# Performance work log

Measured on AMD Instinct MI355X. Metric: run time of the kernel, lower is better.

## Reference

```python
import jax, jax.numpy as jnp
import numpy as np

PATCH_LEN = 16
PATCH_STRIDE = 8
DIM = 512
NUM_HEADS = 8
HEAD_DIM = DIM // NUM_HEADS
NUM_LAYERS = 4
MLP_HIDDEN = 4 * DIM
ROPE_BASE = 10000.0
LN_EPS = 1e-5


def setup_inputs() -> dict:
    key = jax.random.key(0)
    ks = jax.random.split(key, 20)
    B, T, C = 4, 8192, 7
    s = 0.02
    inp = {
        "x": jax.random.normal(ks[0], (B, T, C), dtype=jnp.float32),
        "W_emb": jax.random.normal(ks[1], (PATCH_LEN * C, DIM), dtype=jnp.float32) * s,
        "b_emb": jnp.zeros((DIM,), jnp.float32),
        "ln1_g": jnp.ones((NUM_LAYERS, DIM), jnp.float32),
        "ln1_b": jnp.zeros((NUM_LAYERS, DIM), jnp.float32),
        "W_qkv": jax.random.normal(ks[2], (NUM_LAYERS, DIM, 3 * DIM), dtype=jnp.float32) * s,
        "b_qkv": jnp.zeros((NUM_LAYERS, 3 * DIM), jnp.float32),
        "W_proj": jax.random.normal(ks[3], (NUM_LAYERS, DIM, DIM), dtype=jnp.float32) * s,
        "b_proj": jnp.zeros((NUM_LAYERS, DIM), jnp.float32),
        "ln2_g": jnp.ones((NUM_LAYERS, DIM), jnp.float32),
        "ln2_b": jnp.zeros((NUM_LAYERS, DIM), jnp.float32),
        "W_mlp1": jax.random.normal(ks[4], (NUM_LAYERS, DIM, MLP_HIDDEN), dtype=jnp.float32) * s,
        "b_mlp1": jnp.zeros((NUM_LAYERS, MLP_HIDDEN), jnp.float32),
        "W_mlp2": jax.random.normal(ks[5], (NUM_LAYERS, MLP_HIDDEN, DIM), dtype=jnp.float32) * s,
        "b_mlp2": jnp.zeros((NUM_LAYERS, DIM), jnp.float32),
        "lnf_g": jnp.ones((DIM,), jnp.float32),
        "lnf_b": jnp.zeros((DIM,), jnp.float32),
    }
    return inp


def _layer_norm(x, g, b):
    mu = jnp.mean(x, axis=-1, keepdims=True)
    var = jnp.mean(jnp.square(x - mu), axis=-1, keepdims=True)
    return (x - mu) * jax.lax.rsqrt(var + LN_EPS) * g + b


def _rotate_half(x):
    x1, x2 = jnp.split(x, 2, axis=-1)
    return jnp.concatenate((-x2, x1), axis=-1)


def _rope_cos_sin(seq_len):
    t = jnp.arange(seq_len, dtype=jnp.float32)
    inv_freq = 1.0 / (ROPE_BASE ** (jnp.arange(0, HEAD_DIM, 2, dtype=jnp.float32) / HEAD_DIM))
    freqs = jnp.outer(t, inv_freq)                      # [L, hd/2]
    emb = jnp.concatenate((freqs, freqs), axis=-1)      # [L, hd]
    return jnp.cos(emb), jnp.sin(emb)


def _forward(x, W_emb, b_emb, ln1_g, ln1_b, W_qkv, b_qkv, W_proj, b_proj,
             ln2_g, ln2_b, W_mlp1, b_mlp1, W_mlp2, b_mlp2, lnf_g, lnf_b):
    B, T, C = x.shape
    n = (T - PATCH_LEN) // PATCH_STRIDE + 1
    # torch unfold: [B, n, C, patch_len], then flattened as (C, patch_len)
    idx = jnp.arange(n)[:, None] * PATCH_STRIDE + jnp.arange(PATCH_LEN)[None, :]  # [n, P]
    patches = x[:, idx, :]                              # [B, n, P, C]
    patches = patches.transpose(0, 1, 3, 2).reshape(B, n, C * PATCH_LEN)
    emb = patches @ W_emb + b_emb                       # [B, n, D]

    cos, sin = _rope_cos_sin(n)                         # [n, hd]
    cos = cos[None, None, :, :]
    sin = sin[None, None, :, :]
    scale = HEAD_DIM ** -0.5

    h = emb
    for i in range(NUM_LAYERS):
        # --- attention ---
        y = _layer_norm(h, ln1_g[i], ln1_b[i])
        qkv = (y @ W_qkv[i] + b_qkv[i]).reshape(B, n, 3, NUM_HEADS, HEAD_DIM)
        qkv = qkv.transpose(2, 0, 3, 1, 4)              # [3, B, H, n, hd]
        q, k, v = qkv[0], qkv[1], qkv[2]
        q = q * cos + _rotate_half(q) * sin
        k = k * cos + _rotate_half(k) * sin
        attn = jax.nn.softmax(jnp.einsum('bhqd,bhkd->bhqk', q, k) * scale, axis=-1)
        o = jnp.einsum('bhqk,bhkd->bhqd', attn, v)      # [B, H, n, hd]
        o = o.transpose(0, 2, 1, 3).reshape(B, n, DIM)
        h = h + (o @ W_proj[i] + b_proj[i])
        # --- mlp ---
        y = _layer_norm(h, ln2_g[i], ln2_b[i])
        y = jax.nn.gelu(y @ W_mlp1[i] + b_mlp1[i], approximate=False)
        h = h + (y @ W_mlp2[i] + b_mlp2[i])

    x_out = _layer_norm(h, lnf_g, lnf_b)
    return emb, x_out


def reference(x, W_emb, b_emb, ln1_g, ln1_b, W_qkv, b_qkv, W_proj, b_proj,
              ln2_g, ln2_b, W_mlp1, b_mlp1, W_mlp2, b_mlp2, lnf_g, lnf_b):
    return _forward(x, W_emb, b_emb, ln1_g, ln1_b, W_qkv, b_qkv, W_proj, b_proj,
                    ln2_g, ln2_b, W_mlp1, b_mlp1, W_mlp2, b_mlp2, lnf_g, lnf_b)
```

## Files before the change

### kernel.cpp

```cpp
#include <hip/hip_runtime.h>
#include <hip/hip_bf16.h>
#include <math.h>

#define B_SZ 4
#define T_LEN 8192
#define C_IN 7
#define NPATCH 1023
#define DIM 512
#define NH 8
#define HD 64
#define NLAYERS 4
#define MLP_HID 2048
#define M_ROWS (B_SZ * NPATCH)
#define KEMB 128
#define LN_EPS 1e-5f

typedef __attribute__((ext_vector_type(8))) short short8;
typedef __attribute__((ext_vector_type(4))) float float4v;

static __device__ __forceinline__ unsigned short f2bf(float f) {
  __hip_bfloat16 h = __float2bfloat16(f);
  return *reinterpret_cast<unsigned short*>(&h);
}
static __device__ __forceinline__ float bf2f(unsigned short u) {
  return __uint_as_float(((unsigned)u) << 16);
}

__global__ __launch_bounds__(256) void patch_kernel(
    const float* __restrict__ x, unsigned short* __restrict__ Pm) {
  int idx = blockIdx.x * 256 + threadIdx.x;
  if (idx >= M_ROWS * KEMB) return;
  int row = idx >> 7, c = idx & 127;
  float v = 0.f;
  if (c < 112) {
    int b = row / NPATCH, i = row - b * NPATCH;
    int ci = c >> 4, p = c & 15;
    v = x[((size_t)b * T_LEN + (size_t)i * 8 + p) * C_IN + ci];
  }
  Pm[idx] = f2bf(v);
}

__global__ __launch_bounds__(256) void wemb_cvt_kernel(
    const float* __restrict__ W, unsigned short* __restrict__ Wt) {
  int idx = blockIdx.x * 256 + threadIdx.x;
  if (idx >= DIM * KEMB) return;
  int n = idx >> 7, k = idx & 127;
  float v = (k < 112) ? W[(size_t)k * DIM + n] : 0.f;
  Wt[idx] = f2bf(v);
}

template <bool BF>
__global__ __launch_bounds__(256) void ln_kernel(
    const float* __restrict__ in, const float* __restrict__ g,
    const float* __restrict__ bb, void* __restrict__ outv, int M) {
  int row = blockIdx.x * 4 + (threadIdx.x >> 6);
  if (row >= M) return;
  int lane = threadIdx.x & 63;
  const float* xr = in + (size_t)row * DIM;
  float v[8];
  float s = 0.f;
  #pragma unroll
  for (int k = 0; k < 8; ++k) { v[k] = xr[lane + 64 * k]; s += v[k]; }
  #pragma unroll
  for (int off = 32; off; off >>= 1) s += __shfl_down(s, off);
  s = __shfl(s, 0);
  float mu = s * (1.f / DIM);
  float q = 0.f;
  #pragma unroll
  for (int k = 0; k < 8; ++k) { float d = v[k] - mu; q = fmaf(d, d, q); }
  #pragma unroll
  for (int off = 32; off; off >>= 1) q += __shfl_down(q, off);
  q = __shfl(q, 0);
  float rstd = rsqrtf(q * (1.f / DIM) + LN_EPS);
  #pragma unroll
  for (int k = 0; k < 8; ++k) {
    int d = lane + 64 * k;
    float r = (v[k] - mu) * rstd * g[d] + bb[d];
    if (BF)
      ((unsigned short*)outv)[(size_t)row * DIM + d] = f2bf(r);
    else
      ((float*)outv)[(size_t)row * DIM + d] = r;
  }
}

__global__ __launch_bounds__(256) void wcvt_kernel(
    const float* __restrict__ W, unsigned short* __restrict__ Wt, int K, int N) {
  __shared__ float tile[32][33];
  int n0 = blockIdx.x * 32, k0 = blockIdx.y * 32, L = blockIdx.z;
  const float* Ws = W + (size_t)L * K * N;
  unsigned short* Wd = Wt + (size_t)L * K * N;
  int tx = threadIdx.x & 31, ty = threadIdx.x >> 5;
  #pragma unroll
  for (int i = 0; i < 4; ++i)
    tile[ty + i * 8][tx] = Ws[(size_t)(k0 + ty + i * 8) * N + n0 + tx];
  __syncthreads();
  #pragma unroll
  for (int i = 0; i < 4; ++i)
    Wd[(size_t)(n0 + ty + i * 8) * K + k0 + tx] = f2bf(tile[tx][ty + i * 8]);
}

__global__ __launch_bounds__(256) void rope_tab_kernel(float2* __restrict__ tab) {
  int idx = blockIdx.x * 256 + threadIdx.x;
  if (idx >= NPATCH * 32) return;
  int i = idx >> 5, j = idx & 31;
  float inv = powf(10000.0f, -(float)j * (1.0f / 32.0f));
  float sn, cs;
  sincosf((float)i * inv, &sn, &cs);
  tab[idx] = make_float2(cs, sn);
}

template <int TM, int TN, int EPI>
__global__ __launch_bounds__(256) void mfma_gemm(
    const unsigned short* __restrict__ A, const unsigned short* __restrict__ Bt,
    const float* __restrict__ bias, const float* __restrict__ res,
    float* __restrict__ Cf, float* __restrict__ Cf2,
    unsigned short* __restrict__ Cb, const float2* __restrict__ rtab,
    int M, int N, int K) {
  constexpr int WM = TM / 2, WN = TN / 2;
  constexpr int NI = WM / 16, NJ = WN / 16;
  constexpr int ACH = TM * 4;
  constexpr int TCH = (TM + TN) * 4;
  constexpr int CH = TCH / 256;
  __shared__ __align__(16) unsigned short As[2][TM][40];
  __shared__ __align__(16) unsigned short Bs[2][TN][40];
  const int bm = blockIdx.y * TM;
  const int bn = blockIdx.x * TN;
  const int tid = threadIdx.x;
  const int lane = tid & 63, wave = tid >> 6;
  const int quad = lane >> 4, l16 = lane & 15;
  const int wm = (wave & 1) * WM;
  const int wn = (wave >> 1) * WN;

  float4v acc[NI][NJ];
  #pragma unroll
  for (int i = 0; i < NI; ++i)
    #pragma unroll
    for (int j = 0; j < NJ; ++j)
      acc[i][j] = (float4v){0.f, 0.f, 0.f, 0.f};

  uint4 pr[CH];
  auto load_regs = [&](int kk) {
    #pragma unroll
    for (int it = 0; it < CH; ++it) {
      int c = tid + it * 256;
      if (c < ACH) {
        int row = c >> 2, ch = (c & 3) * 8;
        int gm = bm + row;
        pr[it] = make_uint4(0u, 0u, 0u, 0u);
        if (gm < M) pr[it] = *(const uint4*)(A + (size_t)gm * K + kk + ch);
      } else {
        int c2 = c - ACH;
        int row = c2 >> 2, ch = (c2 & 3) * 8;
        pr[it] = *(const uint4*)(Bt + (size_t)(bn + row) * K + kk + ch);
      }
    }
  };

  load_regs(0);
  int buf = 0;
  for (int k0 = 0; k0 < K; k0 += 32, buf ^= 1) {
    #pragma unroll
    for (int it = 0; it < CH; ++it) {
      int c = tid + it * 256;
      if (c < ACH)
        *(uint4*)&As[buf][c >> 2][(c & 3) * 8] = pr[it];
      else {
        int c2 = c - ACH;
        *(uint4*)&Bs[buf][c2 >> 2][(c2 & 3) * 8] = pr[it];
      }
    }
    if (k0 + 32 < K) load_regs(k0 + 32);
    __syncthreads();
    short8 af[NI], bfr[NJ];
    #pragma unroll
    for (int i = 0; i < NI; ++i)
      af[i] = *(const short8*)&As[buf][wm + i * 16 + l16][quad * 8];
    #pragma unroll
    for (int j = 0; j < NJ; ++j)
      bfr[j] = *(const short8*)&Bs[buf][wn + j * 16 + l16][quad * 8];
    __builtin_amdgcn_s_setprio(1);
    #pragma unroll
    for (int i = 0; i < NI; ++i)
      #pragma unroll
      for (int j = 0; j < NJ; ++j)
        acc[i][j] = __builtin_amdgcn_mfma_f32_16x16x32_bf16(
            af[i], bfr[j], acc[i][j], 0, 0, 0);
    __builtin_amdgcn_s_setprio(0);
  }

  if (EPI == 6) {
    const int sec = (bn + wn) >> 9;
    #pragma unroll
    for (int i = 0; i < NI; ++i) {
      int gm0 = bm + wm + i * 16 + quad * 4;
      #pragma unroll
      for (int r = 0; r < 4; ++r) {
        int gm = gm0 + r;
        if (gm >= M) continue;
        size_t rowoff = (size_t)gm * N;
        if (sec < 2) {
          int ip = gm; if (ip >= 2046) ip -= 2046; if (ip >= 1023) ip -= 1023;
          float sc = (sec == 0) ? 0.125f : 1.f;
          #pragma unroll
          for (int j = 0; j < NJ / 2; ++j) {
            int gn = bn + wn + j * 16 + l16;
            float v0 = acc[i][j][r] + bias[gn];
            float v1 = acc[i][j + NJ / 2][r] + bias[gn + 32];
            float2 t = rtab[ip * 32 + j * 16 + l16];
            Cb[rowoff + gn]      = f2bf((v0 * t.x - v1 * t.y) * sc);
            Cb[rowoff + gn + 32] = f2bf((v1 * t.x + v0 * t.y) * sc);
          }
        } else {
          #pragma unroll
          for (int j = 0; j < NJ; ++j) {
            int gn = bn + wn + j * 16 + l16;
            Cb[rowoff + gn] = f2bf(acc[i][j][r] + bias[gn]);
          }
        }
      }
    }
    return;
  }

  #pragma unroll
  for (int j = 0; j < NJ; ++j) {
    int gn = bn + wn + j * 16 + l16;
    float bv = bias[gn];
    #pragma unroll
    for (int i = 0; i < NI; ++i) {
      int gm0 = bm + wm + i * 16 + quad * 4;
      #pragma unroll
      for (int r = 0; r < 4; ++r) {
        int gm = gm0 + r;
        if (gm < M) {
          float v = acc[i][j][r] + bv;
          size_t off = (size_t)gm * N + gn;
          if (EPI == 1) {
            Cf[off] = v + res[off];
          } else if (EPI == 2) {
            Cb[off] = f2bf(0.5f * v * (1.f + erff(v * 0.70710678118f)));
          } else if (EPI == 3) {
            Cb[off] = f2bf(v);
          } else {
            Cf[off] = v;
            Cf2[off] = v;
          }
        }
      }
    }
  }
}

#define APITCH 72

__global__ __launch_bounds__(256) void attn_kernel(
    const unsigned short* __restrict__ qkvb, unsigned short* __restrict__ o) {
  const int bid = blockIdx.x;
  const int xcd = bid & 7, slot = bid >> 3;
  const int qt0 = (slot & 15) * 64;
  const int gh = xcd + 8 * (slot >> 4);
  const int h = gh & 7, b = gh >> 3;

  const int tid = threadIdx.x;
  const int lane = tid & 63, wave = tid >> 6;
  const int quad = lane >> 4, l16 = lane & 15;

  __shared__ __align__(16) unsigned short Qs[64][APITCH];
  __shared__ __align__(16) unsigned short Ks[2][64][APITCH];
  __shared__ __align__(16) unsigned short Vt[2][HD][APITCH];
  __shared__ __align__(16) unsigned short Ps[4][16][APITCH];

  const int sr = tid >> 2;
  const int sc0 = (tid & 3) * 16;

  {
    int qi = qt0 + sr;
    uint4 a = make_uint4(0u, 0u, 0u, 0u), b2 = a;
    if (qi < NPATCH) {
      const uint4* src = (const uint4*)(qkvb + (size_t)(b * NPATCH + qi) * (3 * DIM) + h * HD + sc0);
      a = src[0]; b2 = src[1];
    }
    *(uint4*)&Qs[sr][sc0] = a;
    *(uint4*)&Qs[sr][sc0 + 8] = b2;
  }

  uint4 pk0, pk1;
  auto load_k = [&](int j0) {
    pk0 = pk1 = make_uint4(0u, 0u, 0u, 0u);
    int j = j0 + sr;
    if (j < NPATCH) {
      const unsigned short* kb = qkvb + (size_t)(b * NPATCH + j) * (3 * DIM) + DIM + h * HD;
      pk0 = *(const uint4*)(kb + sc0);
      pk1 = *(const uint4*)(kb + sc0 + 8);
    }
  };

  const int kp = tid & 31, dg = tid >> 5;
  uint4 pv0, pv1;
  auto load_v = [&](int j0) {
    pv0 = pv1 = make_uint4(0u, 0u, 0u, 0u);
    int j = j0 + 2 * kp;
    const unsigned short* vb = qkvb + (size_t)(b * NPATCH + j) * (3 * DIM) + 2 * DIM + h * HD + dg * 8;
    if (j < NPATCH)     pv0 = *(const uint4*)vb;
    if (j + 1 < NPATCH) pv1 = *(const uint4*)(vb + 3 * DIM);
  };

  load_k(0);
  load_v(0);
  __syncthreads();

  short8 aq0 = *(const short8*)&Qs[wave * 16 + l16][quad * 8];
  short8 aq1 = *(const short8*)&Qs[wave * 16 + l16][32 + quad * 8];

  float4v accO[4];
  #pragma unroll
  for (int j2 = 0; j2 < 4; ++j2) accO[j2] = (float4v){0.f, 0.f, 0.f, 0.f};
  float m_run[4] = {-1e30f, -1e30f, -1e30f, -1e30f};
  float lp[4] = {0.f, 0.f, 0.f, 0.f};

  int buf = 0;
  for (int j0 = 0; j0 < NPATCH; j0 += 64, buf ^= 1) {
    {
      *(uint4*)&Ks[buf][sr][sc0] = pk0;
      *(uint4*)&Ks[buf][sr][sc0 + 8] = pk1;
      unsigned short va[8], vb8[8];
      *(uint4*)&va[0] = pv0;
      *(uint4*)&vb8[0] = pv1;
      #pragma unroll
      for (int u = 0; u < 8; ++u) {
        unsigned pk = (unsigned)va[u] | ((unsigned)vb8[u] << 16);
        *(unsigned*)&Vt[buf][dg * 8 + u][2 * kp] = pk;
      }
    }
    __syncthreads();

    if (j0 + 64 < NPATCH) { load_k(j0 + 64); load_v(j0 + 64); }

    float4v s[4];
    __builtin_amdgcn_s_setprio(1);
    #pragma unroll
    for (int j = 0; j < 4; ++j) {
      s[j] = (float4v){0.f, 0.f, 0.f, 0.f};
      short8 bk0 = *(const short8*)&Ks[buf][j * 16 + l16][quad * 8];
      short8 bk1 = *(const short8*)&Ks[buf][j * 16 + l16][32 + quad * 8];
      s[j] = __builtin_amdgcn_mfma_f32_16x16x32_bf16(aq0, bk0, s[j], 0, 0, 0);
      s[j] = __builtin_amdgcn_mfma_f32_16x16x32_bf16(aq1, bk1, s[j], 0, 0, 0);
    }
    __builtin_amdgcn_s_setprio(0);

    float mx[4];
    #pragma unroll
    for (int r = 0; r < 4; ++r)
      mx[r] = fmaxf(fmaxf(s[0][r], s[1][r]), fmaxf(s[2][r], s[3][r]));
    #pragma unroll
    for (int mask = 1; mask < 16; mask <<= 1)
      #pragma unroll
      for (int r = 0; r < 4; ++r)
        mx[r] = fmaxf(mx[r], __shfl_xor(mx[r], mask));
    float gmax = fmaxf(fmaxf(mx[0] - m_run[0], mx[1] - m_run[1]),
                       fmaxf(mx[2] - m_run[2], mx[3] - m_run[3]));
    if (!__all(gmax <= 8.f)) {
      #pragma unroll
      for (int r = 0; r < 4; ++r) {
        float mnew = fmaxf(m_run[r], mx[r]);
        float al = __expf(m_run[r] - mnew);
        m_run[r] = mnew;
        lp[r] *= al;
        #pragma unroll
        for (int j2 = 0; j2 < 4; ++j2) accO[j2][r] *= al;
      }
    }
    #pragma unroll
    for (int j = 0; j < 4; ++j) {
      bool valid = (j0 + j * 16 + l16) < NPATCH;
      #pragma unroll
      for (int r = 0; r < 4; ++r) {
        float p = valid ? __expf(s[j][r] - m_run[r]) : 0.f;
        lp[r] += p;
        Ps[wave][quad * 4 + r][j * 16 + l16] = f2bf(p);
      }
    }

    short8 pa0 = *(const short8*)&Ps[wave][l16][quad * 8];
    short8 pa1 = *(const short8*)&Ps[wave][l16][32 + quad * 8];
    __builtin_amdgcn_s_setprio(1);
    #pragma unroll
    for (int j2 = 0; j2 < 4; ++j2) {
      short8 v0 = *(const short8*)&Vt[buf][j2 * 16 + l16][quad * 8];
      short8 v1 = *(const short8*)&Vt[buf][j2 * 16 + l16][32 + quad * 8];
      accO[j2] = __builtin_amdgcn_mfma_f32_16x16x32_bf16(pa0, v0, accO[j2], 0, 0, 0);
      accO[j2] = __builtin_amdgcn_mfma_f32_16x16x32_bf16(pa1, v1, accO[j2], 0, 0, 0);
    }
    __builtin_amdgcn_s_setprio(0);
  }

  #pragma unroll
  for (int mask = 1; mask < 16; mask <<= 1)
    #pragma unroll
    for (int r = 0; r < 4; ++r)
      lp[r] += __shfl_xor(lp[r], mask);

  #pragma unroll
  for (int r = 0; r < 4; ++r) {
    int qi = qt0 + wave * 16 + quad * 4 + r;
    if (qi < NPATCH) {
      float inv = 1.f / lp[r];
      size_t off = (size_t)(b * NPATCH + qi) * DIM + h * HD + l16;
      #pragma unroll
      for (int j2 = 0; j2 < 4; ++j2)
        o[off + j2 * 16] = f2bf(accO[j2][r] * inv);
    }
  }
}

extern "C" void kernel_launch(void* const* d_in, const int* in_sizes, int n_in,
                              void* d_out, int out_size, void* d_ws, size_t ws_size,
                              hipStream_t stream) {
  const float* x      = (const float*)d_in[0];
  const float* W_emb  = (const float*)d_in[1];
  const float* b_emb  = (const float*)d_in[2];
  const float* ln1_g  = (const float*)d_in[3];
  const float* ln1_b  = (const float*)d_in[4];
  const float* W_qkv  = (const float*)d_in[5];
  const float* b_qkv  = (const float*)d_in[6];
  const float* W_proj = (const float*)d_in[7];
  const float* b_proj = (const float*)d_in[8];
  const float* ln2_g  = (const float*)d_in[9];
  const float* ln2_b  = (const float*)d_in[10];
  const float* W_mlp1 = (const float*)d_in[11];
  const float* b_mlp1 = (const float*)d_in[12];
  const float* W_mlp2 = (const float*)d_in[13];
  const float* b_mlp2 = (const float*)d_in[14];
  const float* lnf_g  = (const float*)d_in[15];
  const float* lnf_b  = (const float*)d_in[16];
  float* out = (float*)d_out;

  float* h              = (float*)d_ws;
  unsigned short* qkvb  = (unsigned short*)(h + (size_t)M_ROWS * DIM);
  unsigned short* midbf = qkvb;
  unsigned short* ybf   = qkvb + (size_t)M_ROWS * MLP_HID;
  unsigned short* obf   = ybf;
  unsigned short* wqkv_t  = ybf + (size_t)M_ROWS * DIM;
  unsigned short* wproj_t = wqkv_t  + (size_t)NLAYERS * DIM * 3 * DIM;
  unsigned short* wmlp1_t = wproj_t + (size_t)NLAYERS * DIM * DIM;
  unsigned short* wmlp2_t = wmlp1_t + (size_t)NLAYERS * DIM * MLP_HID;
  float2* rtab = (float2*)(wmlp2_t + (size_t)NLAYERS * MLP_HID * DIM);
  unsigned short* Pm    = (unsigned short*)(rtab + (size_t)NPATCH * 32);
  unsigned short* Wembt = Pm + (size_t)M_ROWS * KEMB;

  wcvt_kernel<<<dim3(3 * DIM / 32, DIM / 32, NLAYERS), 256, 0, stream>>>(W_qkv,  wqkv_t,  DIM, 3 * DIM);
  wcvt_kernel<<<dim3(DIM / 32, DIM / 32, NLAYERS),     256, 0, stream>>>(W_proj, wproj_t, DIM, DIM);
  wcvt_kernel<<<dim3(MLP_HID / 32, DIM / 32, NLAYERS), 256, 0, stream>>>(W_mlp1, wmlp1_t, DIM, MLP_HID);
  wcvt_kernel<<<dim3(DIM / 32, MLP_HID / 32, NLAYERS), 256, 0, stream>>>(W_mlp2, wmlp2_t, MLP_HID, DIM);
  rope_tab_kernel<<<(NPATCH * 32 + 255) / 256, 256, 0, stream>>>(rtab);
  patch_kernel<<<(M_ROWS * KEMB + 255) / 256, 256, 0, stream>>>(x, Pm);
  wemb_cvt_kernel<<<(DIM * KEMB + 255) / 256, 256, 0, stream>>>(W_emb, Wembt);

  const int MT64 = (M_ROWS + 63) / 64;
  const int MT128 = (M_ROWS + 127) / 128;
  const int LNG = (M_ROWS + 3) / 4;

  mfma_gemm<64, 64, 5><<<dim3(DIM / 64, MT64), 256, 0, stream>>>(
      Pm, Wembt, b_emb, nullptr, out, h, nullptr, nullptr, M_ROWS, DIM, KEMB);

  for (int L = 0; L < NLAYERS; ++L) {
    ln_kernel<true><<<LNG, 256, 0, stream>>>(h, ln1_g + L * DIM, ln1_b + L * DIM, ybf, M_ROWS);
    mfma_gemm<128, 128, 6><<<dim3(3 * DIM / 128, MT128), 256, 0, stream>>>(
        ybf, wqkv_t + (size_t)L * DIM * 3 * DIM, b_qkv + L * 3 * DIM,
        nullptr, nullptr, nullptr, qkvb, rtab, M_ROWS, 3 * DIM, DIM);
    attn_kernel<<<dim3(512), 256, 0, stream>>>(qkvb, obf);
    mfma_gemm<64, 64, 1><<<dim3(DIM / 64, MT64), 256, 0, stream>>>(
        obf, wproj_t + (size_t)L * DIM * DIM, b_proj + L * DIM,
        h, h, nullptr, nullptr, nullptr, M_ROWS, DIM, DIM);
    ln_kernel<true><<<LNG, 256, 0, stream>>>(h, ln2_g + L * DIM, ln2_b + L * DIM, ybf, M_ROWS);
    mfma_gemm<128, 128, 2><<<dim3(MLP_HID / 128, MT128), 256, 0, stream>>>(
        ybf, wmlp1_t + (size_t)L * DIM * MLP_HID, b_mlp1 + L * MLP_HID,
        nullptr, nullptr, nullptr, midbf, nullptr, M_ROWS, MLP_HID, DIM);
    mfma_gemm<64, 64, 1><<<dim3(DIM / 64, MT64), 256, 0, stream>>>(
        midbf, wmlp2_t + (size_t)L * MLP_HID * DIM, b_mlp2 + L * DIM,
        h, h, nullptr, nullptr, nullptr, M_ROWS, DIM, MLP_HID);
  }

  ln_kernel<false><<<LNG, 256, 0, stream>>>(h, lnf_g, lnf_b, out + (size_t)M_ROWS * DIM, M_ROWS);
}
```

Baseline: 692.9 us.

## Split attention KV range across two wave groups with final softmax merge

The attention kernel now launches 512 threads per block. Two halves of four waves each process alternate 64-key chunks of a 128-key tile, then merge their partial max, sum and output through shared memory. Q fragments are loaded straight from global memory into registers instead of being staged through shared memory. The aim is more waves in flight per block and shorter serial KV loops. In exchange it removes the previous double-buffered prefetch overlap, adds an extra barrier per iteration, and adds a final cross-half reduction.

```diff
diff --git a/kernel.cpp b/kernel.cpp
--- a/kernel.cpp
+++ b/kernel.cpp
@@ -253,7 +253,7 @@
 
 #define APITCH 72
 
-__global__ __launch_bounds__(256) void attn_kernel(
+__global__ __launch_bounds__(512, 4) void attn_kernel(
     const unsigned short* __restrict__ qkvb, unsigned short* __restrict__ o) {
   const int bid = blockIdx.x;
   const int xcd = bid & 7, slot = bid >> 3;
@@ -264,53 +264,40 @@
   const int tid = threadIdx.x;
   const int lane = tid & 63, wave = tid >> 6;
   const int quad = lane >> 4, l16 = lane & 15;
-
-  __shared__ __align__(16) unsigned short Qs[64][APITCH];
+  const int half = wave >> 2, wq = wave & 3;
+
   __shared__ __align__(16) unsigned short Ks[2][64][APITCH];
-  __shared__ __align__(16) unsigned short Vt[2][HD][APITCH];
-  __shared__ __align__(16) unsigned short Ps[4][16][APITCH];
-
-  const int sr = tid >> 2;
-  const int sc0 = (tid & 3) * 16;
-
+  __shared__ __align__(16) unsigned short Vt[2][64][APITCH];
+  __shared__ __align__(16) unsigned short Ps[8][16][APITCH];
+
+  short8 aq0 = {0, 0, 0, 0, 0, 0, 0, 0}, aq1 = aq0;
   {
-    int qi = qt0 + sr;
-    uint4 a = make_uint4(0u, 0u, 0u, 0u), b2 = a;
-    if (qi < NPATCH) {
-      const uint4* src = (const uint4*)(qkvb + (size_t)(b * NPATCH + qi) * (3 * DIM) + h * HD + sc0);
-      a = src[0]; b2 = src[1];
-    }
-    *(uint4*)&Qs[sr][sc0] = a;
-    *(uint4*)&Qs[sr][sc0 + 8] = b2;
-  }
-
-  uint4 pk0, pk1;
-  auto load_k = [&](int j0) {
-    pk0 = pk1 = make_uint4(0u, 0u, 0u, 0u);
-    int j = j0 + sr;
-    if (j < NPATCH) {
-      const unsigned short* kb = qkvb + (size_t)(b * NPATCH + j) * (3 * DIM) + DIM + h * HD;
-      pk0 = *(const uint4*)(kb + sc0);
-      pk1 = *(const uint4*)(kb + sc0 + 8);
-    }
+    int qrow = qt0 + wq * 16 + l16;
+    if (qrow < NPATCH) {
+      const uint4* qr = (const uint4*)(qkvb + (size_t)(b * NPATCH + qrow) * (3 * DIM) + h * HD + quad * 8);
+      aq0 = __builtin_bit_cast(short8, qr[0]);
+      aq1 = __builtin_bit_cast(short8, qr[4]);
+    }
+  }
+
+  const int krow = tid >> 2, kc0 = (tid & 3) * 16;
+  const int kp2 = tid & 63, dg = tid >> 6;
+  uint4 pk0, pk1, pv0, pv1;
+  auto load_kv = [&](int js) {
+    pk0 = pk1 = pv0 = pv1 = make_uint4(0u, 0u, 0u, 0u);
+    int jk = js + krow;
+    if (jk < NPATCH) {
+      const unsigned short* kb = qkvb + (size_t)(b * NPATCH + jk) * (3 * DIM) + DIM + h * HD;
+      pk0 = *(const uint4*)(kb + kc0);
+      pk1 = *(const uint4*)(kb + kc0 + 8);
+    }
+    int jv = js + 2 * kp2;
+    const unsigned short* vb = qkvb + (size_t)(b * NPATCH + jv) * (3 * DIM) + 2 * DIM + h * HD + dg * 8;
+    if (jv < NPATCH)     pv0 = *(const uint4*)vb;
+    if (jv + 1 < NPATCH) pv1 = *(const uint4*)(vb + 3 * DIM);
   };
 
-  const int kp = tid & 31, dg = tid >> 5;
-  uint4 pv0, pv1;
-  auto load_v = [&](int j0) {
-    pv0 = pv1 = make_uint4(0u, 0u, 0u, 0u);
-    int j = j0 + 2 * kp;
-    const unsigned short* vb = qkvb + (size_t)(b * NPATCH + j) * (3 * DIM) + 2 * DIM + h * HD + dg * 8;
-    if (j < NPATCH)     pv0 = *(const uint4*)vb;
-    if (j + 1 < NPATCH) pv1 = *(const uint4*)(vb + 3 * DIM);
-  };
-
-  load_k(0);
-  load_v(0);
-  __syncthreads();
-
-  short8 aq0 = *(const short8*)&Qs[wave * 16 + l16][quad * 8];
-  short8 aq1 = *(const short8*)&Qs[wave * 16 + l16][32 + quad * 8];
+  load_kv(0);
 
   float4v accO[4];
   #pragma unroll
@@ -318,31 +305,34 @@
   float m_run[4] = {-1e30f, -1e30f, -1e30f, -1e30f};
   float lp[4] = {0.f, 0.f, 0.f, 0.f};
 
-  int buf = 0;
-  for (int j0 = 0; j0 < NPATCH; j0 += 64, buf ^= 1) {
+  constexpr int NIT = (NPATCH + 127) / 128;
+  for (int it = 0; it < NIT; ++it) {
+    if (it > 0) __syncthreads();
     {
-      *(uint4*)&Ks[buf][sr][sc0] = pk0;
-      *(uint4*)&Ks[buf][sr][sc0 + 8] = pk1;
+      *(uint4*)&Ks[krow >> 6][krow & 63][kc0] = pk0;
+      *(uint4*)&Ks[krow >> 6][krow & 63][kc0 + 8] = pk1;
       unsigned short va[8], vb8[8];
       *(uint4*)&va[0] = pv0;
       *(uint4*)&vb8[0] = pv1;
+      const int vh = kp2 >> 5, lp2 = kp2 & 31;
       #pragma unroll
       for (int u = 0; u < 8; ++u) {
         unsigned pk = (unsigned)va[u] | ((unsigned)vb8[u] << 16);
-        *(unsigned*)&Vt[buf][dg * 8 + u][2 * kp] = pk;
+        *(unsigned*)&Vt[vh][dg * 8 + u][2 * lp2] = pk;
       }
     }
     __syncthreads();
-
-    if (j0 + 64 < NPATCH) { load_k(j0 + 64); load_v(j0 + 64); }
+    if (it + 1 < NIT) load_kv((it + 1) * 128);
+
+    const int j0 = it * 128 + half * 64;
 
     float4v s[4];
     __builtin_amdgcn_s_setprio(1);
     #pragma unroll
     for (int j = 0; j < 4; ++j) {
       s[j] = (float4v){0.f, 0.f, 0.f, 0.f};
-      short8 bk0 = *(const short8*)&Ks[buf][j * 16 + l16][quad * 8];
-      short8 bk1 = *(const short8*)&Ks[buf][j * 16 + l16][32 + quad * 8];
+      short8 bk0 = *(const short8*)&Ks[half][j * 16 + l16][quad * 8];
+      short8 bk1 = *(const short8*)&Ks[half][j * 16 + l16][32 + quad * 8];
       s[j] = __builtin_amdgcn_mfma_f32_16x16x32_bf16(aq0, bk0, s[j], 0, 0, 0);
       s[j] = __builtin_amdgcn_mfma_f32_16x16x32_bf16(aq1, bk1, s[j], 0, 0, 0);
     }
@@ -386,8 +376,8 @@
     __builtin_amdgcn_s_setprio(1);
     #pragma unroll
     for (int j2 = 0; j2 < 4; ++j2) {
-      short8 v0 = *(const short8*)&Vt[buf][j2 * 16 + l16][quad * 8];
-      short8 v1 = *(const short8*)&Vt[buf][j2 * 16 + l16][32 + quad * 8];
+      short8 v0 = *(const short8*)&Vt[half][j2 * 16 + l16][quad * 8];
+      short8 v1 = *(const short8*)&Vt[half][j2 * 16 + l16][32 + quad * 8];
       accO[j2] = __builtin_amdgcn_mfma_f32_16x16x32_bf16(pa0, v0, accO[j2], 0, 0, 0);
       accO[j2] = __builtin_amdgcn_mfma_f32_16x16x32_bf16(pa1, v1, accO[j2], 0, 0, 0);
     }
@@ -400,15 +390,40 @@
     for (int r = 0; r < 4; ++r)
       lp[r] += __shfl_xor(lp[r], mask);
 
-  #pragma unroll
-  for (int r = 0; r < 4; ++r) {
-    int qi = qt0 + wave * 16 + quad * 4 + r;
-    if (qi < NPATCH) {
-      float inv = 1.f / lp[r];
-      size_t off = (size_t)(b * NPATCH + qi) * DIM + h * HD + l16;
-      #pragma unroll
-      for (int j2 = 0; j2 < 4; ++j2)
-        o[off + j2 * 16] = f2bf(accO[j2][r] * inv);
+  float* Pf = (float*)&Ps[0][0][0];
+  __syncthreads();
+  if (half == 1) {
+    #pragma unroll
+    for (int j2 = 0; j2 < 4; ++j2)
+      #pragma unroll
+      for (int r = 0; r < 4; ++r)
+        Pf[((wq * 64 + lane) << 4) + j2 * 4 + r] = accO[j2][r];
+    if (l16 == 0) {
+      #pragma unroll
+      for (int r = 0; r < 4; ++r) {
+        Pf[4096 + ((wq * 16 + quad * 4 + r) << 1)]     = m_run[r];
+        Pf[4096 + ((wq * 16 + quad * 4 + r) << 1) + 1] = lp[r];
+      }
+    }
+  }
+  __syncthreads();
+  if (half == 0) {
+    #pragma unroll
+    for (int r = 0; r < 4; ++r) {
+      float m1 = Pf[4096 + ((wq * 16 + quad * 4 + r) << 1)];
+      float l1 = Pf[4096 + ((wq * 16 + quad * 4 + r) << 1) + 1];
+      float M = fmaxf(m_run[r], m1);
+      float w0 = __expf(m_run[r] - M), w1 = __expf(m1 - M);
+      float inv = 1.f / (w0 * lp[r] + w1 * l1);
+      int qi = qt0 + wq * 16 + quad * 4 + r;
+      if (qi < NPATCH) {
+        size_t off = (size_t)(b * NPATCH + qi) * DIM + h * HD + l16;
+        #pragma unroll
+        for (int j2 = 0; j2 < 4; ++j2) {
+          float a1 = Pf[((wq * 64 + lane) << 4) + j2 * 4 + r];
+          o[off + j2 * 16] = f2bf((w0 * accO[j2][r] + w1 * a1) * inv);
+        }
+      }
     }
   }
 }
@@ -468,7 +483,7 @@
     mfma_gemm<128, 128, 6><<<dim3(3 * DIM / 128, MT128), 256, 0, stream>>>(
         ybf, wqkv_t + (size_t)L * DIM * 3 * DIM, b_qkv + L * 3 * DIM,
         nullptr, nullptr, nullptr, qkvb, rtab, M_ROWS, 3 * DIM, DIM);
-    attn_kernel<<<dim3(512), 256, 0, stream>>>(qkvb, obf);
+    attn_kernel<<<dim3(512), 512, 0, stream>>>(qkvb, obf);
     mfma_gemm<64, 64, 1><<<dim3(DIM / 64, MT64), 256, 0, stream>>>(
         obf, wproj_t + (size_t)L * DIM * DIM, b_proj + L * DIM,
         h, h, nullptr, nullptr, nullptr, M_ROWS, DIM, DIM);
```

New measurement: 683.9 us. About the same (-1.3%).
